# Kernel optimization log

Hardware: AMD Instinct MI355X
Metric: run time of the kernel (lower is better)

The kernel has to match this reference:

```python
import jax, jax.numpy as jnp
import numpy as np

IN_F = 4096
OUT_F = 4096
GROUP = 128                      # quantization group size
NG = IN_F * OUT_F // GROUP       # 131072 groups
LORA_R = 16
LORA_SCALE = 32.0 / 16.0         # lora_alpha / lora_r


def _dequant(indices, codebook, scales):
    # Unpack two INT4 nibbles per byte: low nibble first, then high (interleaved).
    low = indices & 15
    high = (indices >> 4) & 15
    idx = jnp.stack([low, high], axis=1).reshape(-1)          # [numel]
    # Codebook lookup, per-group scaling.
    vals = codebook[idx].reshape(NG, GROUP) * scales[:, None]  # [NG, GROUP]
    return vals.reshape(OUT_F, IN_F)


def setup_inputs() -> dict:
    key = jax.random.key(0)
    ks = jax.random.split(key, 7)
    return {
        "x": jax.random.normal(ks[0], (4, 2048, IN_F), dtype=jnp.float32),
        "indices": jax.random.randint(ks[1], (IN_F * OUT_F // 2,), 0, 256, dtype=jnp.int32),
        "codebook": jax.random.normal(ks[2], (16,), dtype=jnp.float32),
        "scales": jax.random.uniform(ks[3], (NG,), dtype=jnp.float32, minval=0.01, maxval=1.0),
        "lora_A": jax.random.normal(ks[4], (IN_F, LORA_R), dtype=jnp.float32) / 64.0,
        "lora_B": jax.random.normal(ks[5], (LORA_R, OUT_F), dtype=jnp.float32) / 64.0,
        "bias": jax.random.normal(ks[6], (OUT_F,), dtype=jnp.float32),
    }


def reference(x, indices, codebook, scales, lora_A, lora_B, bias):
    # lowram path: dequantize INT4 codebook weights, F.linear, fused LoRA add, bias.
    W = _dequant(indices, codebook, scales)                    # [OUT_F, IN_F]
    h = jnp.einsum('bsi,oi->bso', x, W)                        # F.linear (no bias yet)
    h = h + (x @ lora_A) @ lora_B * LORA_SCALE                 # LoRA adapter (dropout=0)
    return h + bias
```

## Files before the change

### kernel.cpp

```cpp
#include <hip/hip_runtime.h>
#include <stdint.h>

#define IN_F   4096
#define OUT_F  4096
#define M_TOT  8192
#define KDIM   4096

typedef float          f32x4  __attribute__((ext_vector_type(4)));
typedef int            i32x4  __attribute__((ext_vector_type(4)));
typedef unsigned short u16x8  __attribute__((ext_vector_type(8)));
typedef __bf16         bf16x8 __attribute__((ext_vector_type(8)));

__device__ __forceinline__ unsigned short f2bf(float f) {
  uint32_t u = __builtin_bit_cast(uint32_t, f);
  u = (u + 0x7FFFu + ((u >> 16) & 1u)) >> 16;
  return (unsigned short)u;
}
__device__ __forceinline__ float bf2f(unsigned short s) {
  return __builtin_bit_cast(float, (uint32_t)s << 16);
}

__device__ __forceinline__ void gld_lds16(const void* g, void* l) {
  __builtin_amdgcn_global_load_lds((const __attribute__((address_space(1))) void*)g,
                                   (__attribute__((address_space(3))) void*)l,
                                   16, 0, 0);
}

__global__ __launch_bounds__(256) void k_xcast(const f32x4* __restrict__ x,
                                               u16x8* __restrict__ xb) {
  int t = blockIdx.x * 256 + threadIdx.x;
  f32x4 a = x[2 * t];
  f32x4 b = x[2 * t + 1];
  u16x8 o;
  o[0] = f2bf(a[0]); o[1] = f2bf(a[1]); o[2] = f2bf(a[2]); o[3] = f2bf(a[3]);
  o[4] = f2bf(b[0]); o[5] = f2bf(b[1]); o[6] = f2bf(b[2]); o[7] = f2bf(b[3]);
  xb[t] = o;
}

__global__ __launch_bounds__(256) void k_lora(const float* __restrict__ A,
                                              const float* __restrict__ Bm,
                                              unsigned short* __restrict__ L) {
  __shared__ float sB[16][64];
  const int ib = blockIdx.x * 256;
  const int ob = blockIdx.y * 64;
  const int t  = threadIdx.x;
  for (int j = 0; j < 4; ++j) {
    int idx = t + j * 256;
    int r = idx >> 6, oc = idx & 63;
    sB[r][oc] = Bm[r * OUT_F + ob + oc];
  }
  float a[16];
  const f32x4* Ap = (const f32x4*)(A + (size_t)(ib + t) * 16);
  #pragma unroll
  for (int j = 0; j < 4; ++j) {
    f32x4 v = Ap[j];
    a[4*j+0] = v[0]; a[4*j+1] = v[1]; a[4*j+2] = v[2]; a[4*j+3] = v[3];
  }
  __syncthreads();
  unsigned short* Lp = L + (size_t)ob * IN_F + ib + t;
  #pragma unroll 4
  for (int oc = 0; oc < 64; ++oc) {
    float acc = 0.f;
    #pragma unroll
    for (int r = 0; r < 16; ++r) acc += a[r] * sB[r][oc];
    Lp[(size_t)oc * IN_F] = f2bf(acc * 2.0f);
  }
}

__global__ __launch_bounds__(256) void k_dequant(const int* __restrict__ idx,
                                                 const float* __restrict__ cb,
                                                 const float* __restrict__ scales,
                                                 const unsigned short* __restrict__ L,
                                                 unsigned short* __restrict__ Wc) {
  __shared__ float scb[16];
  const int t = blockIdx.x * 256 + threadIdx.x;
  if (threadIdx.x < 16) scb[threadIdx.x] = cb[threadIdx.x];
  __syncthreads();
  i32x4 w = ((const i32x4*)idx)[t];
  float sc = scales[t >> 4];
  u16x8 lw = ((const u16x8*)L)[t];
  u16x8 o;
  #pragma unroll
  for (int j = 0; j < 4; ++j) {
    int word = w[j];
    float v0 = scb[word & 15] * sc + bf2f(lw[2 * j]);
    float v1 = scb[(word >> 4) & 15] * sc + bf2f(lw[2 * j + 1]);
    o[2 * j]     = f2bf(v0);
    o[2 * j + 1] = f2bf(v1);
  }
  ((u16x8*)Wc)[t] = o;
}


#define BARR()  __builtin_amdgcn_s_barrier()
#define LGKM0() asm volatile("s_waitcnt lgkmcnt(0)" ::: "memory")
#define VMC6()  asm volatile("s_waitcnt vmcnt(6)" ::: "memory")
#define VMC0()  asm volatile("s_waitcnt vmcnt(0)" ::: "memory")

#define STAGE_A(kt, ha, c) do {                                                          \
  gld_lds16(Ag + (size_t)((ha) * 128) * KDIM + (kt) * 64,                                \
            smem + (c) * 32768 + (ha) * 16384 + ldsw);                                   \
  gld_lds16(Ag + (size_t)((ha) * 128 + 64) * KDIM + (kt) * 64,                           \
            smem + (c) * 32768 + (ha) * 16384 + 8192 + ldsw);                            \
} while (0)

#define STAGE_B(kt, hb, c) do {                                                          \
  gld_lds16(Bg + (size_t)((hb) * 128) * KDIM + (kt) * 64,                                \
            smem + 65536 + (c) * 32768 + (hb) * 16384 + ldsw);                           \
  gld_lds16(Bg + (size_t)((hb) * 128 + 64) * KDIM + (kt) * 64,                           \
            smem + 65536 + (c) * 32768 + (hb) * 16384 + 8192 + ldsw);                    \
} while (0)

#define LOAD_A(qm, c) do {                                                               \
  const char* _p = smem + (c) * 32768 + rowA + (qm) * 8192;                              \
  _Pragma("unroll")                                                                      \
  for (int mi = 0; mi < 4; ++mi) {                                                       \
    af[mi][0] = *(const bf16x8*)(_p + mi * 2048 + coff0);                                \
    af[mi][1] = *(const bf16x8*)(_p + mi * 2048 + coff1);                                \
  }                                                                                      \
} while (0)

#define LOAD_B(c) do {                                                                   \
  const char* _p = smem + 65536 + (c) * 32768 + rowB;                                    \
  _Pragma("unroll")                                                                      \
  for (int ni = 0; ni < 4; ++ni) {                                                       \
    bfr[ni][0] = *(const bf16x8*)(_p + ni * 2048 + coff0);                               \
    bfr[ni][1] = *(const bf16x8*)(_p + ni * 2048 + coff1);                               \
  }                                                                                      \
} while (0)

#define MFMA_PH(qm, nb) do {                                                             \
  __builtin_amdgcn_s_setprio(1);                                                         \
  _Pragma("unroll")                                                                      \
  for (int mi = 0; mi < 4; ++mi)                                                         \
    _Pragma("unroll")                                                                    \
    for (int nj = 0; nj < 2; ++nj)                                                       \
      _Pragma("unroll")                                                                  \
      for (int kk = 0; kk < 2; ++kk)                                                     \
        acc[(qm) * 4 + mi][(nb) * 2 + nj] = __builtin_amdgcn_mfma_f32_16x16x32_bf16(     \
            af[mi][kk], bfr[(nb) * 2 + nj][kk], acc[(qm) * 4 + mi][(nb) * 2 + nj],       \
            0, 0, 0);                                                                    \
  __builtin_amdgcn_s_setprio(0);                                                         \
} while (0)

#define TILE(t_, c_, doS4, doS123, VMCODE) do {                                          \
                                                                                \
  LOAD_A(0, c_); LOAD_B(c_);                                                             \
  if (doS4) STAGE_A((t_) + 1, 1, (c_) ^ 1);                                              \
  BARR(); LGKM0(); MFMA_PH(0, 0); BARR();                                                \
                                                                                \
  if (doS123) STAGE_B((t_) + 2, 0, c_);                                                  \
  BARR(); MFMA_PH(0, 1); BARR();                                                         \
                                                                                \
  LOAD_A(1, c_);                                                                         \
  if (doS123) STAGE_B((t_) + 2, 1, c_);                                                  \
  BARR(); LGKM0(); MFMA_PH(1, 1); BARR();                                                \
                                                                                \
  if (doS123) STAGE_A((t_) + 2, 0, c_);                                                  \
  BARR(); MFMA_PH(1, 0); VMCODE; BARR();                                                 \
} while (0)

__global__ __launch_bounds__(512, 2) void k_gemm(const unsigned short* __restrict__ A,
                                                 const unsigned short* __restrict__ B,
                                                 const float* __restrict__ bias,
                                                 float* __restrict__ C) {
  __shared__ char smem[131072];
  const int tid  = threadIdx.x;
  const int lane = tid & 63;
  const int wv   = tid >> 6;
  const int wm   = wv >> 2;
  const int wn   = wv & 3;
  const int r    = lane & 15;
  const int q    = lane >> 4;
  const int xr   = r & 7;
  const int coff0 = (q ^ xr) << 4;
  const int coff1 = ((q + 4) ^ xr) << 4;
  const int rowA = (wm * 128 + r) * 128;
  const int rowB = (wn * 64 + r) * 128;
  const int srow = tid >> 3;
  const int scol = ((tid & 7) ^ ((tid >> 3) & 7)) * 8;
  const int ldsw = wv * 1024;
  const int bm = blockIdx.x;
  const int bn = blockIdx.y;

  const unsigned short* Ag = A + (size_t)(bm * 256 + srow) * KDIM + scol;
  const unsigned short* Bg = B + (size_t)(bn * 256 + srow) * KDIM + scol;

  bf16x8 af[4][2], bfr[4][2];
  f32x4 acc[8][4];
  #pragma unroll
  for (int m = 0; m < 8; ++m)
    #pragma unroll
    for (int n = 0; n < 4; ++n)
      acc[m][n] = (f32x4){0.f, 0.f, 0.f, 0.f};

  STAGE_B(0, 0, 0); STAGE_B(0, 1, 0); STAGE_A(0, 0, 0); STAGE_A(0, 1, 0);
  STAGE_B(1, 0, 1); STAGE_B(1, 1, 1); STAGE_A(1, 0, 1);
  VMC6();
  BARR();

  #pragma unroll 1
  for (int t = 0; t < 62; t += 2) {
    TILE(t,     0, 1, 1, VMC6());
    TILE(t + 1, 1, 1, 1, VMC6());
  }
  TILE(62, 0, 1, 0, VMC0());
  TILE(63, 1, 0, 0, VMC0());

  __syncthreads();
  {
    char* eps = smem + wv * 4096;
    const int row0 = bm * 256 + wm * 128;
    const int col0 = bn * 256 + wn * 64;
    const f32x4 bias4 = *(const f32x4*)(bias + col0 + r * 4);
    #pragma unroll
    for (int mi = 0; mi < 8; ++mi) {
      #pragma unroll
      for (int j = 0; j < 4; ++j)
        #pragma unroll
        for (int ni = 0; ni < 4; ++ni)
          *(float*)(eps + (((q * 4 + j) * 64) + ni * 16 + r) * 4) = acc[mi][ni][j];
      LGKM0();
      __builtin_amdgcn_sched_barrier(0);
      #pragma unroll
      for (int p = 0; p < 4; ++p) {
        const int row = p * 4 + q;
        f32x4 v = *(const f32x4*)(eps + row * 256 + r * 16);
        v[0] += bias4[0]; v[1] += bias4[1]; v[2] += bias4[2]; v[3] += bias4[3];
        *(f32x4*)(C + (size_t)(row0 + mi * 16 + row) * OUT_F + col0 + r * 4) = v;
      }
      asm volatile("" ::: "memory");
    }
  }
}

extern "C" void kernel_launch(void* const* d_in, const int* in_sizes, int n_in,
                              void* d_out, int out_size, void* d_ws, size_t ws_size,
                              hipStream_t stream) {
  const float* x    = (const float*)d_in[0];
  const int*   idx  = (const int*)d_in[1];
  const float* cb   = (const float*)d_in[2];
  const float* scl  = (const float*)d_in[3];
  const float* lA   = (const float*)d_in[4];
  const float* lB   = (const float*)d_in[5];
  const float* bias = (const float*)d_in[6];
  float* out = (float*)d_out;

  unsigned short* xb = (unsigned short*)d_ws;
  unsigned short* Wc = (unsigned short*)((char*)d_ws + (size_t)M_TOT * KDIM * 2);
  unsigned short* Lbuf = (unsigned short*)d_out;

  k_xcast<<<16384, 256, 0, stream>>>((const f32x4*)x, (u16x8*)xb);
  k_lora<<<dim3(16, 64), 256, 0, stream>>>(lA, lB, Lbuf);
  k_dequant<<<8192, 256, 0, stream>>>(idx, cb, scl, Lbuf, Wc);
  k_gemm<<<dim3(32, 16), 512, 0, stream>>>(xb, Wc, bias, out);
}
```

Measured before the change: 282.6 us.

## Replace phased 8-wave GEMM schedule with simple double-buffered prefetch loop

Replaces the hand-interleaved four-phase tile schedule, with its barriers, partial vmcnt waits and two-tile-ahead staging, with a plain double-buffer loop. Each iteration issues the full next-tile global-to-LDS loads up front, reads both A halves and B from LDS into separate registers, runs all MFMAs, then waits for all memory and takes one barrier. This cuts barrier count and scheduling complexity but gives up the finer overlap and prefetch depth, raises register pressure through the extra A fragment array, and fully drains vmcnt every tile.

```diff
diff --git a/kernel.cpp b/kernel.cpp
--- a/kernel.cpp
+++ b/kernel.cpp
@@ -94,7 +94,6 @@
 
 #define BARR()  __builtin_amdgcn_s_barrier()
 #define LGKM0() asm volatile("s_waitcnt lgkmcnt(0)" ::: "memory")
-#define VMC6()  asm volatile("s_waitcnt vmcnt(6)" ::: "memory")
 #define VMC0()  asm volatile("s_waitcnt vmcnt(0)" ::: "memory")
 
 #define STAGE_A(kt, ha, c) do {                                                          \
@@ -111,12 +110,12 @@
             smem + 65536 + (c) * 32768 + (hb) * 16384 + 8192 + ldsw);                    \
 } while (0)
 
-#define LOAD_A(qm, c) do {                                                               \
+#define LOAD_AH(DST, qm, c) do {                                                         \
   const char* _p = smem + (c) * 32768 + rowA + (qm) * 8192;                              \
   _Pragma("unroll")                                                                      \
   for (int mi = 0; mi < 4; ++mi) {                                                       \
-    af[mi][0] = *(const bf16x8*)(_p + mi * 2048 + coff0);                                \
-    af[mi][1] = *(const bf16x8*)(_p + mi * 2048 + coff1);                                \
+    DST[mi][0] = *(const bf16x8*)(_p + mi * 2048 + coff0);                               \
+    DST[mi][1] = *(const bf16x8*)(_p + mi * 2048 + coff1);                               \
   }                                                                                      \
 } while (0)
 
@@ -129,7 +128,7 @@
   }                                                                                      \
 } while (0)
 
-#define MFMA_PH(qm, nb) do {                                                             \
+#define MFMA_PH(qm, nb, AF) do {                                                         \
   __builtin_amdgcn_s_setprio(1);                                                         \
   _Pragma("unroll")                                                                      \
   for (int mi = 0; mi < 4; ++mi)                                                         \
@@ -138,26 +137,20 @@
       _Pragma("unroll")                                                                  \
       for (int kk = 0; kk < 2; ++kk)                                                     \
         acc[(qm) * 4 + mi][(nb) * 2 + nj] = __builtin_amdgcn_mfma_f32_16x16x32_bf16(     \
-            af[mi][kk], bfr[(nb) * 2 + nj][kk], acc[(qm) * 4 + mi][(nb) * 2 + nj],       \
+            AF[mi][kk], bfr[(nb) * 2 + nj][kk], acc[(qm) * 4 + mi][(nb) * 2 + nj],       \
             0, 0, 0);                                                                    \
   __builtin_amdgcn_s_setprio(0);                                                         \
 } while (0)
 
-#define TILE(t_, c_, doS4, doS123, VMCODE) do {                                          \
-                                                                                \
-  LOAD_A(0, c_); LOAD_B(c_);                                                             \
-  if (doS4) STAGE_A((t_) + 1, 1, (c_) ^ 1);                                              \
-  BARR(); LGKM0(); MFMA_PH(0, 0); BARR();                                                \
-                                                                                \
-  if (doS123) STAGE_B((t_) + 2, 0, c_);                                                  \
-  BARR(); MFMA_PH(0, 1); BARR();                                                         \
-                                                                                \
-  LOAD_A(1, c_);                                                                         \
-  if (doS123) STAGE_B((t_) + 2, 1, c_);                                                  \
-  BARR(); LGKM0(); MFMA_PH(1, 1); BARR();                                                \
-                                                                                \
-  if (doS123) STAGE_A((t_) + 2, 0, c_);                                                  \
-  BARR(); MFMA_PH(1, 0); VMCODE; BARR();                                                 \
+#define TILE2(t_, c_, doStage) do {                                                      \
+  if (doStage) {                                                                         \
+    STAGE_B((t_) + 1, 0, (c_) ^ 1); STAGE_B((t_) + 1, 1, (c_) ^ 1);                      \
+    STAGE_A((t_) + 1, 0, (c_) ^ 1); STAGE_A((t_) + 1, 1, (c_) ^ 1);                      \
+  }                                                                                      \
+  LOAD_AH(afA, 0, c_); LOAD_B(c_); LOAD_AH(afB, 1, c_);                                  \
+  MFMA_PH(0, 0, afA); MFMA_PH(0, 1, afA);                                                \
+  MFMA_PH(1, 1, afB); MFMA_PH(1, 0, afB);                                                \
+  LGKM0(); VMC0(); BARR();                                                               \
 } while (0)
 
 __global__ __launch_bounds__(512, 2) void k_gemm(const unsigned short* __restrict__ A,
@@ -186,7 +179,7 @@
   const unsigned short* Ag = A + (size_t)(bm * 256 + srow) * KDIM + scol;
   const unsigned short* Bg = B + (size_t)(bn * 256 + srow) * KDIM + scol;
 
-  bf16x8 af[4][2], bfr[4][2];
+  bf16x8 afA[4][2], afB[4][2], bfr[4][2];
   f32x4 acc[8][4];
   #pragma unroll
   for (int m = 0; m < 8; ++m)
@@ -195,17 +188,16 @@
       acc[m][n] = (f32x4){0.f, 0.f, 0.f, 0.f};
 
   STAGE_B(0, 0, 0); STAGE_B(0, 1, 0); STAGE_A(0, 0, 0); STAGE_A(0, 1, 0);
-  STAGE_B(1, 0, 1); STAGE_B(1, 1, 1); STAGE_A(1, 0, 1);
-  VMC6();
+  VMC0();
   BARR();
 
   #pragma unroll 1
   for (int t = 0; t < 62; t += 2) {
-    TILE(t,     0, 1, 1, VMC6());
-    TILE(t + 1, 1, 1, 1, VMC6());
-  }
-  TILE(62, 0, 1, 0, VMC0());
-  TILE(63, 1, 0, 0, VMC0());
+    TILE2(t,     0, 1);
+    TILE2(t + 1, 1, 1);
+  }
+  TILE2(62, 0, 1);
+  TILE2(63, 1, 0);
 
   __syncthreads();
   {
```

New measurement: 280.5 us. No clear change (-0.7%).
